# Kernel tuning notes

Hardware: AMD Instinct MI355X
Metric: run time of the kernel (lower is better)

## Reference

```python
import jax, jax.numpy as jnp
import numpy as np

B, S, D, F, H, R, BLK = 1, 2048, 1024, 2816, 16, 16, 64
DH = D // H  # 64

# bitsandbytes NF4 codebook
NF4_CODE = jnp.array([-1.0, -0.6961928009986877, -0.5250730514526367, -0.39491748809814453,
                      -0.28444138169288635, -0.18477343022823334, -0.09105003625154495, 0.0,
                      0.07958029955625534, 0.16093020141124725, 0.24611230194568634, 0.33791524171829224,
                      0.44070982933044434, 0.5626170039176941, 0.7229568362236023, 1.0], dtype=jnp.float32)


def dequant_nf4(codes, absmax, shape):
    # blockwise NF4 dequant: codebook lookup * per-64-element absmax scale
    w = NF4_CODE[codes.reshape(-1)]
    return (w.reshape(-1, BLK) * absmax[:, None]).reshape(shape)


def rmsnorm(x, w, eps=1e-10):
    return x * jax.lax.rsqrt(jnp.mean(x * x, axis=-1, keepdims=True) + eps) * w


def rotate_half(x):
    x1, x2 = jnp.split(x, 2, axis=-1)
    return jnp.concatenate((-x2, x1), axis=-1)


def apply_rope(x, cos, sin, pos):
    # x: [B,H,S,DH], pos: [B,S] -> gather rope tables per position
    c = cos[pos][:, None]  # [B,1,S,DH]
    s = sin[pos][:, None]
    return x * c + rotate_half(x) * s


def proj(x, codes, absmax, la, lb, shape):
    # fused NF4 dequant-matmul + additive LoRA branch: x @ W.T + (x @ A) @ B
    w = dequant_nf4(codes, absmax, shape)
    return x @ w.T + (x @ la) @ lb


def _forward(x, nw1, nw2, cos, sin,
             qa, qla, qlb, ka, kla, klb, va, vla, vlb, oa, ola, olb,
             ga, gla, glb, ua, ula, ulb, da, dla, dlb,
             pos, qc, kc, vc, oc, gc, uc, dc):
    h1 = rmsnorm(x, nw1)
    q = proj(h1, qc, qa, qla, qlb, (D, D))
    k = proj(h1, kc, ka, kla, klb, (D, D))
    v = proj(h1, vc, va, vla, vlb, (D, D))

    def heads(t):
        return t.reshape(B, S, H, DH).transpose(0, 2, 1, 3)

    q = apply_rope(heads(q), cos, sin, pos)
    k = apply_rope(heads(k), cos, sin, pos)
    v = heads(v)

    scores = jnp.einsum('bhqd,bhkd->bhqk', q, k) / np.float32(np.sqrt(DH))
    causal = jnp.tril(jnp.ones((S, S), dtype=bool))
    mask = jnp.where(causal, 0.0, -1e9).astype(scores.dtype)  # additive attention_mask
    attn = jax.nn.softmax(scores + mask, axis=-1)
    o = jnp.einsum('bhqk,bhkd->bhqd', attn, v).transpose(0, 2, 1, 3).reshape(B, S, D)
    o = proj(o, oc, oa, ola, olb, (D, D))

    x1 = x + o  # first residual
    h2 = rmsnorm(x1, nw2)
    gate = proj(h2, gc, ga, gla, glb, (F, D))
    up = proj(h2, uc, ua, ula, ulb, (F, D))
    had = up * jax.nn.silu(gate)  # SwiGLU hadamard
    down = proj(had, dc, da, dla, dlb, (D, F))
    return x1 + down


def setup_inputs():
    ks = iter(jax.random.split(jax.random.key(0), 48))

    def rn(shape, scale=1.0):
        return jax.random.normal(next(ks), shape, jnp.float32) * scale

    def cd(shape):
        return jax.random.randint(next(ks), shape, 0, 16, dtype=jnp.int32)

    def am(n):
        return jax.random.uniform(next(ks), (n,), jnp.float32) * 0.04 + 0.01

    inp = {'x': rn((B, S, D)),
           'norm_weight_1': 1.0 + rn((D,), 0.02),
           'norm_weight_2': 1.0 + rn((D,), 0.02)}
    inv = 1.0 / (10000.0 ** (jnp.arange(0, DH, 2, dtype=jnp.float32) / DH))
    ang = jnp.arange(S, dtype=jnp.float32)[:, None] * inv[None, :]
    emb = jnp.concatenate((ang, ang), axis=-1)  # [S, DH]
    inp['cos'], inp['sin'] = jnp.cos(emb), jnp.sin(emb)
    inp['position_ids'] = jnp.broadcast_to(jnp.arange(S, dtype=jnp.int32), (B, S))
    shapes = {'q': (D, D), 'k': (D, D), 'v': (D, D), 'o': (D, D),
              'gate': (F, D), 'up': (F, D), 'down': (D, F)}
    for p, (o, i) in shapes.items():
        inp['w_%s_codes' % p] = cd((o, i))
        inp['w_%s_absmax' % p] = am(o * i // BLK)
        inp['w_%s_lora_a' % p] = rn((i, R), 1.0 / np.sqrt(i))
        inp['w_%s_lora_b' % p] = rn((R, o), 0.01)
    return inp


def reference(x, norm_weight_1, norm_weight_2, cos, sin, position_ids,
              w_q_codes, w_q_absmax, w_q_lora_a, w_q_lora_b,
              w_k_codes, w_k_absmax, w_k_lora_a, w_k_lora_b,
              w_v_codes, w_v_absmax, w_v_lora_a, w_v_lora_b,
              w_o_codes, w_o_absmax, w_o_lora_a, w_o_lora_b,
              w_gate_codes, w_gate_absmax, w_gate_lora_a, w_gate_lora_b,
              w_up_codes, w_up_absmax, w_up_lora_a, w_up_lora_b,
              w_down_codes, w_down_absmax, w_down_lora_a, w_down_lora_b):
    return _forward(x, norm_weight_1, norm_weight_2, cos, sin,
                    w_q_absmax, w_q_lora_a, w_q_lora_b,
                    w_k_absmax, w_k_lora_a, w_k_lora_b,
                    w_v_absmax, w_v_lora_a, w_v_lora_b,
                    w_o_absmax, w_o_lora_a, w_o_lora_b,
                    w_gate_absmax, w_gate_lora_a, w_gate_lora_b,
                    w_up_absmax, w_up_lora_a, w_up_lora_b,
                    w_down_absmax, w_down_lora_a, w_down_lora_b,
                    position_ids, w_q_codes, w_k_codes, w_v_codes,
                    w_o_codes, w_gate_codes, w_up_codes, w_down_codes)
```

## Files before the change

### kernel.cpp

```cpp
#include <hip/hip_runtime.h>
#include <stdint.h>


#define Sq   2048
#define Dm   1024
#define Fm   2816
#define Hh   16
#define KE1  1088
#define KE2  1088
#define LGW  1088
#define KE3  2880
#define NQKV 3072
#define NGU  5632

typedef short bf16x8 __attribute__((ext_vector_type(8)));
typedef float f32x4  __attribute__((ext_vector_type(4)));

__constant__ float NF4_LUT[16] = {
    -1.0f, -0.6961928009986877f, -0.5250730514526367f, -0.39491748809814453f,
    -0.28444138169288635f, -0.18477343022823334f, -0.09105003625154495f, 0.0f,
    0.07958029955625534f, 0.16093020141124725f, 0.24611230194568634f,
    0.33791524171829224f, 0.44070982933044434f, 0.5626170039176941f,
    0.7229568362236023f, 1.0f};

__device__ inline unsigned short f2bf(float f) {
    union { float f; uint32_t u; } v; v.f = f;
    uint32_t u = v.u;
    return (unsigned short)((u + 0x7FFFu + ((u >> 16) & 1u)) >> 16);
}
__device__ inline float bf2f(unsigned short h) {
    union { uint32_t u; float f; } v; v.u = ((uint32_t)h) << 16;
    return v.f;
}
__device__ inline unsigned short truncbf(float f) {
    union { float f; uint32_t u; } v; v.f = f;
    return (unsigned short)(v.u >> 16);
}

#define GLD16(gp, lp)                                                         \
    __builtin_amdgcn_global_load_lds(                                         \
        (__attribute__((address_space(1))) void*)(uintptr_t)(gp),             \
        (__attribute__((address_space(3))) void*)(uint32_t)(uintptr_t)(lp),   \
        16, 0, 0)

__global__ __launch_bounds__(256) void rmsnorm_ext(
    const float* __restrict__ X, const float* __restrict__ W,
    unsigned short* Hout, int ldh)
{
    int s = blockIdx.x, tid = threadIdx.x;
    const float4 v = *(const float4*)(X + (size_t)s * Dm + tid * 4);
    float ss = v.x * v.x + v.y * v.y + v.z * v.z + v.w * v.w;
#pragma unroll
    for (int m = 1; m < 64; m <<= 1) ss += __shfl_xor(ss, m);
    __shared__ float red[4];
    int lane = tid & 63, wave = tid >> 6;
    if (lane == 0) red[wave] = ss;
    __syncthreads();
    float scale = rsqrtf((red[0] + red[1] + red[2] + red[3]) * (1.0f / Dm) + 1e-10f);
    const float4 w = *(const float4*)(W + tid * 4);
    alignas(8) unsigned short o[4];
    o[0] = f2bf(v.x * scale * w.x);
    o[1] = f2bf(v.y * scale * w.y);
    o[2] = f2bf(v.z * scale * w.z);
    o[3] = f2bf(v.w * scale * w.w);
    *(ushort4*)(Hout + (size_t)s * ldh + tid * 4) = *(ushort4*)o;
    if (tid < 64) Hout[(size_t)s * ldh + Dm + tid] = 0;
}

__device__ inline void dq_row8(const float* lut, const int* cod, const float* am,
                               const float* lb, int nr, int c8, int K, int Nlb,
                               int toff, unsigned short* out)
{
    if (c8 < K) {
        size_t base = (size_t)nr * K + c8;
        const int4* cp = (const int4*)(cod + base);
        int4 ca = cp[0], cb = cp[1];
        float a = am[base >> 6];
        out[0] = f2bf(lut[ca.x] * a); out[1] = f2bf(lut[ca.y] * a);
        out[2] = f2bf(lut[ca.z] * a); out[3] = f2bf(lut[ca.w] * a);
        out[4] = f2bf(lut[cb.x] * a); out[5] = f2bf(lut[cb.y] * a);
        out[6] = f2bf(lut[cb.z] * a); out[7] = f2bf(lut[cb.w] * a);
    } else {
        int r = c8 - toff;
#pragma unroll
        for (int i = 0; i < 8; ++i) out[i] = 0;
        if (r >= 0 && r < 16) {
#pragma unroll
            for (int i = 0; i < 8; ++i) out[i] = f2bf(lb[(size_t)(r + i) * Nlb + nr]);
        }
    }
}

__global__ __launch_bounds__(256) void prep_weights(
    const int* __restrict__ qc, const int* __restrict__ kc, const int* __restrict__ vc,
    const int* __restrict__ oc, const int* __restrict__ gc, const int* __restrict__ uc,
    const int* __restrict__ dc,
    const float* __restrict__ qa, const float* __restrict__ ka, const float* __restrict__ va,
    const float* __restrict__ oa, const float* __restrict__ ga, const float* __restrict__ ua,
    const float* __restrict__ da,
    const float* __restrict__ qla, const float* __restrict__ kla, const float* __restrict__ vla,
    const float* __restrict__ ola, const float* __restrict__ gla, const float* __restrict__ ula,
    const float* __restrict__ dla,
    const float* __restrict__ qlb, const float* __restrict__ klb, const float* __restrict__ vlb,
    const float* __restrict__ olb, const float* __restrict__ glb, const float* __restrict__ ulb,
    const float* __restrict__ dlb,
    const float* __restrict__ x, const float* __restrict__ nw1,
    unsigned short* __restrict__ lapk, unsigned short* __restrict__ Wq,
    unsigned short* __restrict__ Wo, unsigned short* __restrict__ Wgu,
    unsigned short* __restrict__ Wd, unsigned short* __restrict__ h)
{
    int b = blockIdx.x, tid = threadIdx.x;
    if (b >= 6678) {
        int s = b - 6678;
        const float4 v = *(const float4*)(x + (size_t)s * Dm + tid * 4);
        float ss = v.x * v.x + v.y * v.y + v.z * v.z + v.w * v.w;
#pragma unroll
        for (int m = 1; m < 64; m <<= 1) ss += __shfl_xor(ss, m);
        __shared__ float red[4];
        int lane = tid & 63, wave = tid >> 6;
        if (lane == 0) red[wave] = ss;
        __syncthreads();
        float scale = rsqrtf((red[0] + red[1] + red[2] + red[3]) * (1.0f / Dm) + 1e-10f);
        const float4 w = *(const float4*)(nw1 + tid * 4);
        alignas(8) unsigned short o[4];
        o[0] = f2bf(v.x * scale * w.x);
        o[1] = f2bf(v.y * scale * w.y);
        o[2] = f2bf(v.z * scale * w.z);
        o[3] = f2bf(v.w * scale * w.w);
        *(ushort4*)(h + (size_t)s * KE1 + tid * 4) = *(ushort4*)o;
        if (tid < 64) h[(size_t)s * KE1 + Dm + tid] = 0;
        return;
    }
    if (b < 70) {
        int chunk = b * 4 + (tid >> 6);
        int lane = tid & 63;
        int lr = lane & 15, quad = lane >> 4;
        const float* la;
        int lc;
        if (chunk < 192) {
            int m = chunk >> 5; lc = chunk & 31;
            la = (m == 0) ? qla : (m == 1) ? kla : (m == 2) ? vla
               : (m == 3) ? ola : (m == 4) ? gla : ula;
        } else {
            la = dla; lc = chunk - 192;
        }
        alignas(16) unsigned short out[8];
#pragma unroll
        for (int e = 0; e < 8; ++e)
            out[e] = f2bf(la[(size_t)(lc * 32 + quad * 8 + e) * 16 + lr]);
        *(uint4*)(lapk + (size_t)chunk * 512 + lane * 8) = *(uint4*)out;
        return;
    }
    __shared__ float lut[16];
    if (tid < 16) lut[tid] = NF4_LUT[tid];
    __syncthreads();
    if (b < 1702) {
        int idx = (b - 70) * 256 + tid;
        int n = idx / 136;
        int c8 = (idx - n * 136) * 8;
        int seg = n >> 10, nr = n & 1023;
        const int* cod   = (seg == 0) ? qc : (seg == 1) ? kc : vc;
        const float* am  = (seg == 0) ? qa : (seg == 1) ? ka : va;
        const float* lb  = (seg == 0) ? qlb : (seg == 1) ? klb : vlb;
        int toff = 1024 + (seg << 4);
        alignas(16) unsigned short out[8];
        dq_row8(lut, cod, am, lb, nr, c8, 1024, 1024, toff, out);
        *(uint4*)(Wq + (size_t)n * KE1 + c8) = *(uint4*)out;
    } else if (b < 2246) {
        int idx = (b - 1702) * 256 + tid;
        int n = idx / 136;
        int c8 = (idx - n * 136) * 8;
        alignas(16) unsigned short out[8];
        dq_row8(lut, oc, oa, olb, n, c8, 1024, Dm, 1024, out);
        *(uint4*)(Wo + (size_t)n * KE2 + c8) = *(uint4*)out;
    } else if (b < 5238) {
        int idx = (b - 2246) * 256 + tid;
        int n = idx / 136;
        int v8 = idx - n * 136;
        int m = n >> 1, mat = n & 1;
        const int* cod  = mat ? uc : gc;
        const float* am = mat ? ua : ga;
        const float* lb = mat ? ulb : glb;
        int toff = 1024 + (mat << 4);
        alignas(16) unsigned short out[8];
        dq_row8(lut, cod, am, lb, m, v8 * 8, 1024, Fm, toff, out);
        int ch = v8 >> 2, sub = v8 & 3;
        int ph = ch + (n % 34); if (ph >= 34) ph -= 34;
        *(uint4*)(Wgu + (size_t)n * LGW + ph * 32 + sub * 8) = *(uint4*)out;
    } else {
        int idx = (b - 5238) * 256 + tid;
        int n = idx / 360;
        if (n >= Dm) return;
        int c8 = (idx - n * 360) * 8;
        alignas(16) unsigned short out[8];
        dq_row8(lut, dc, da, dlb, n, c8, 2816, Dm, 2816, out);
        *(uint4*)(Wd + (size_t)n * KE3 + c8) = *(uint4*)out;
    }
}

template<int NM>
__global__ __launch_bounds__(256) void lora_mfma(
    unsigned short* Aext, int lda, int K,
    const unsigned short* __restrict__ lapk, int c0, int c1, int c2,
    int toff, int zoff, int zn)
{
    int tid = threadIdx.x;
    int lane = tid & 63, wave = tid >> 6;
    int lr = lane & 15, quad = lane >> 4;
    int r0 = blockIdx.x * 16;
    int nc4 = K >> 7;
    int gc0 = wave * nc4;
    const unsigned short* Ab = Aext + (size_t)(r0 + lr) * lda + quad * 8;
    int cb[3] = {c0, c1, c2};
    f32x4 zero = {0.f, 0.f, 0.f, 0.f};
    f32x4 acc[NM];
#pragma unroll
    for (int m = 0; m < NM; ++m) acc[m] = zero;
    for (int cc = 0; cc < nc4; ++cc) {
        int gc = gc0 + cc;
        bf16x8 af = *(const bf16x8*)(Ab + gc * 32);
#pragma unroll
        for (int m = 0; m < NM; ++m) {
            bf16x8 bf = *(const bf16x8*)(lapk + (size_t)(cb[m] + gc) * 512 + lane * 8);
            acc[m] = __builtin_amdgcn_mfma_f32_16x16x32_bf16(af, bf, acc[m], 0, 0, 0);
        }
    }
    __shared__ float red[3][NM * 64 * 4];
    if (wave > 0) {
#pragma unroll
        for (int m = 0; m < NM; ++m)
#pragma unroll
            for (int r = 0; r < 4; ++r)
                red[wave - 1][(m * 64 + lane) * 4 + r] = acc[m][r];
    }
    __syncthreads();
    if (wave == 0) {
#pragma unroll
        for (int m = 0; m < NM; ++m)
#pragma unroll
            for (int r = 0; r < 4; ++r)
                acc[m][r] += red[0][(m * 64 + lane) * 4 + r]
                           + red[1][(m * 64 + lane) * 4 + r]
                           + red[2][(m * 64 + lane) * 4 + r];
#pragma unroll
        for (int r = 0; r < 4; ++r) {
            int row = r0 + quad * 4 + r;
#pragma unroll
            for (int m = 0; m < NM; ++m)
                Aext[(size_t)row * lda + toff + m * 16 + lr] = f2bf(acc[m][r]);
        }
        if (zn > 0) {
            int row = r0 + lr, j0 = quad * 4;
            for (int j = j0; j < zn; j += 64) {
                alignas(8) unsigned short z4[4] = {0, 0, 0, 0};
                *(ushort4*)(Aext + (size_t)row * lda + zoff + j) = *(ushort4*)z4;
            }
        }
    }
}

__global__ __launch_bounds__(256) void gemm128(
    const unsigned short* __restrict__ A, int lda,
    const unsigned short* __restrict__ B, int ldb, int K,
    unsigned short* __restrict__ Cb, int ldc)
{
    __shared__ __align__(16) unsigned short At[2][128 * 32];
    __shared__ __align__(16) unsigned short Bt[2][128 * 32];
    int tid = threadIdx.x;
    int lane = tid & 63, wave = tid >> 6;
    int lr = lane & 15, quad = lane >> 4;
    int wm = (wave >> 1) * 64, wn = (wave & 1) * 64;
    int row0 = blockIdx.y * 128, col0 = blockIdx.x * 128;
    f32x4 acc[4][4];
    f32x4 zero = {0.f, 0.f, 0.f, 0.f};
#pragma unroll
    for (int i = 0; i < 4; ++i)
#pragma unroll
        for (int j = 0; j < 4; ++j) acc[i][j] = zero;
    int sw = ((tid & 3) ^ ((tid >> 3) & 3)) * 8;
    const unsigned short* Ag  = A + (size_t)(row0 + (tid >> 2)) * lda + sw;
    const unsigned short* Ag2 = Ag + (size_t)64 * lda;
    const unsigned short* Bg  = B + (size_t)(col0 + (tid >> 2)) * ldb + sw;
    const unsigned short* Bg2 = Bg + (size_t)64 * ldb;
    int l0 = tid * 8, l1 = (tid + 256) * 8;
    GLD16(Ag, At[0] + l0); GLD16(Ag2, At[0] + l1);
    GLD16(Bg, Bt[0] + l0); GLD16(Bg2, Bt[0] + l1);
    int sq = (quad ^ ((lr >> 1) & 3)) * 8;
    int nIter = K >> 5;
    for (int it = 0; it < nIter; ++it) {
        int cur = it & 1;
        __syncthreads();
        if (it + 1 < nIter) {
            int k = (it + 1) << 5, nx = cur ^ 1;
            GLD16(Ag + k, At[nx] + l0); GLD16(Ag2 + k, At[nx] + l1);
            GLD16(Bg + k, Bt[nx] + l0); GLD16(Bg2 + k, Bt[nx] + l1);
        }
        bf16x8 af[4], bfr[4];
#pragma unroll
        for (int i = 0; i < 4; ++i)
            af[i] = *(const bf16x8*)(At[cur] + (wm + i * 16 + lr) * 32 + sq);
#pragma unroll
        for (int j = 0; j < 4; ++j)
            bfr[j] = *(const bf16x8*)(Bt[cur] + (wn + j * 16 + lr) * 32 + sq);
#pragma unroll
        for (int i = 0; i < 4; ++i)
#pragma unroll
            for (int j = 0; j < 4; ++j)
                acc[i][j] = __builtin_amdgcn_mfma_f32_16x16x32_bf16(af[i], bfr[j], acc[i][j], 0, 0, 0);
    }
#pragma unroll
    for (int i = 0; i < 4; ++i) {
        int rowb = row0 + wm + i * 16 + quad * 4;
#pragma unroll
        for (int j = 0; j < 4; ++j) {
            int col = col0 + wn + j * 16 + lr;
#pragma unroll
            for (int r = 0; r < 4; ++r)
                Cb[(size_t)(rowb + r) * ldc + col] = f2bf(acc[i][j][r]);
        }
    }
}

__global__ __launch_bounds__(256) void gemm_gu(
    const unsigned short* __restrict__ A, int lda,
    const unsigned short* __restrict__ B, int ldb, int K,
    unsigned short* __restrict__ Hb)
{
    __shared__ __align__(16) unsigned short At[2][128 * 32];
    __shared__ __align__(16) unsigned short Bt[2][128 * 32];
    int tid = threadIdx.x;
    int lane = tid & 63, wave = tid >> 6;
    int lr = lane & 15, quad = lane >> 4;
    int wm = (wave >> 1) * 64, wn = (wave & 1) * 64;
    int row0 = blockIdx.y * 128, col0 = blockIdx.x * 128;
    f32x4 acc[4][4];
    f32x4 zero = {0.f, 0.f, 0.f, 0.f};
#pragma unroll
    for (int i = 0; i < 4; ++i)
#pragma unroll
        for (int j = 0; j < 4; ++j) acc[i][j] = zero;
    int sw = ((tid & 3) ^ ((tid >> 3) & 3)) * 8;
    const unsigned short* Ag  = A + (size_t)(row0 + (tid >> 2)) * lda + sw;
    const unsigned short* Ag2 = Ag + (size_t)64 * lda;
    int rB  = col0 + (tid >> 2);
    const unsigned short* Bb  = B + (size_t)rB * ldb + sw;
    const unsigned short* Bb2 = B + (size_t)(rB + 64) * ldb + sw;
    int cB  = rB % 34;
    int cB2 = (rB + 64) % 34;
    int l0 = tid * 8, l1 = (tid + 256) * 8;
    GLD16(Ag, At[0] + l0); GLD16(Ag2, At[0] + l1);
    GLD16(Bb + cB * 32, Bt[0] + l0);
    GLD16(Bb2 + cB2 * 32, Bt[0] + l1);
    cB  = (cB + 1 == 34) ? 0 : cB + 1;
    cB2 = (cB2 + 1 == 34) ? 0 : cB2 + 1;
    int sq = (quad ^ ((lr >> 1) & 3)) * 8;
    int nIter = K >> 5;
    for (int it = 0; it < nIter; ++it) {
        int cur = it & 1;
        __syncthreads();
        if (it + 1 < nIter) {
            int k = (it + 1) << 5, nx = cur ^ 1;
            GLD16(Ag + k, At[nx] + l0); GLD16(Ag2 + k, At[nx] + l1);
            GLD16(Bb + cB * 32, Bt[nx] + l0);
            GLD16(Bb2 + cB2 * 32, Bt[nx] + l1);
            cB  = (cB + 1 == 34) ? 0 : cB + 1;
            cB2 = (cB2 + 1 == 34) ? 0 : cB2 + 1;
        }
        bf16x8 af[4], bfr[4];
#pragma unroll
        for (int i = 0; i < 4; ++i)
            af[i] = *(const bf16x8*)(At[cur] + (wm + i * 16 + lr) * 32 + sq);
#pragma unroll
        for (int j = 0; j < 4; ++j)
            bfr[j] = *(const bf16x8*)(Bt[cur] + (wn + j * 16 + lr) * 32 + sq);
#pragma unroll
        for (int i = 0; i < 4; ++i)
#pragma unroll
            for (int j = 0; j < 4; ++j)
                acc[i][j] = __builtin_amdgcn_mfma_f32_16x16x32_bf16(af[i], bfr[j], acc[i][j], 0, 0, 0);
    }
#pragma unroll
    for (int i = 0; i < 4; ++i) {
        int rowb = row0 + wm + i * 16 + quad * 4;
#pragma unroll
        for (int j = 0; j < 4; ++j) {
            int col = col0 + wn + j * 16 + lr;
#pragma unroll
            for (int r = 0; r < 4; ++r) {
                float own = acc[i][j][r];
                float oth = __shfl_xor(own, 1);
                if (!(lr & 1)) {
                    float sig = 1.0f / (1.0f + __expf(-own));
                    Hb[(size_t)(rowb + r) * KE3 + (col >> 1)] = f2bf(oth * own * sig);
                }
            }
        }
    }
}

template<int TAG>
__global__ __launch_bounds__(256) void gemm_s(
    const unsigned short* __restrict__ A, int lda,
    const unsigned short* __restrict__ B, int ldb, int K,
    float* __restrict__ Cf, int ldc, const float* __restrict__ Radd)
{
    __shared__ __align__(16) unsigned short At[2][64 * 64];
    __shared__ __align__(16) unsigned short Bt[2][64 * 64];
    int tid = threadIdx.x;
    int lane = tid & 63, wave = tid >> 6;
    int lr = lane & 15, quad = lane >> 4;
    int row0 = blockIdx.y * 64, col0 = blockIdx.x * 64;
    f32x4 acc[4];
    f32x4 zero = {0.f, 0.f, 0.f, 0.f};
#pragma unroll
    for (int j = 0; j < 4; ++j) acc[j] = zero;
    int rs = tid >> 3;
    int g8 = ((tid & 7) ^ (rs & 7)) * 8;
    const unsigned short* Ag  = A + (size_t)(row0 + rs) * lda + g8;
    const unsigned short* Ag2 = Ag + (size_t)32 * lda;
    const unsigned short* Bg  = B + (size_t)(col0 + rs) * ldb + g8;
    const unsigned short* Bg2 = Bg + (size_t)32 * ldb;
    int l0 = tid * 8, l1 = (tid + 256) * 8;
    GLD16(Ag, At[0] + l0); GLD16(Ag2, At[0] + l1);
    GLD16(Bg, Bt[0] + l0); GLD16(Bg2, Bt[0] + l1);
    int c0 = (quad ^ (lr & 7)) * 8;
    int c1 = ((4 + quad) ^ (lr & 7)) * 8;
    int nIter = K >> 6;
    for (int it = 0; it < nIter; ++it) {
        int cur = it & 1;
        __syncthreads();
        if (it + 1 < nIter) {
            int k = (it + 1) << 6, nx = cur ^ 1;
            GLD16(Ag + k, At[nx] + l0); GLD16(Ag2 + k, At[nx] + l1);
            GLD16(Bg + k, Bt[nx] + l0); GLD16(Bg2 + k, Bt[nx] + l1);
        }
        const unsigned short* arow = At[cur] + (wave * 16 + lr) * 64;
        bf16x8 a0 = *(const bf16x8*)(arow + c0);
        bf16x8 a1 = *(const bf16x8*)(arow + c1);
        bf16x8 b0[4], b1[4];
#pragma unroll
        for (int j = 0; j < 4; ++j) {
            const unsigned short* brow = Bt[cur] + (j * 16 + lr) * 64;
            b0[j] = *(const bf16x8*)(brow + c0);
            b1[j] = *(const bf16x8*)(brow + c1);
        }
#pragma unroll
        for (int j = 0; j < 4; ++j) {
            acc[j] = __builtin_amdgcn_mfma_f32_16x16x32_bf16(a0, b0[j], acc[j], 0, 0, 0);
            acc[j] = __builtin_amdgcn_mfma_f32_16x16x32_bf16(a1, b1[j], acc[j], 0, 0, 0);
        }
    }
    int rowb = row0 + wave * 16 + quad * 4;
#pragma unroll
    for (int j = 0; j < 4; ++j) {
        int col = col0 + j * 16 + lr;
#pragma unroll
        for (int r = 0; r < 4; ++r) {
            size_t o = (size_t)(rowb + r) * ldc + col;
            Cf[o] = acc[j][r] + Radd[o];
        }
    }
}

__global__ __launch_bounds__(256) void rope_pack(
    const unsigned short* __restrict__ qkv,
    const float* __restrict__ cosT, const float* __restrict__ sinT,
    const int* __restrict__ pos,
    unsigned short* __restrict__ kpk, unsigned short* __restrict__ vpk)
{
    int b = blockIdx.x, tid = threadIdx.x;
    if (b < 1024) {
        int g = b * 256 + tid;
        int lr = g & 15, quad = (g >> 4) & 3, cch = (g >> 6) & 1;
        int t = (g >> 7) & 127, h = g >> 14;
        int s = t * 16 + lr;
        int p = pos[s];
        int d0 = cch * 32 + quad * 8;
        const unsigned short* krow = qkv + (size_t)s * NQKV + Dm + h * 64;
        uint4 kv8 = *(const uint4*)(krow + d0);
        uint4 kp8 = *(const uint4*)(krow + ((d0 + 32) & 63));
        float sgn = (d0 < 32) ? -1.f : 1.f;
        const float* cp = cosT + p * 64 + d0;
        const float* sp = sinT + p * 64 + d0;
        const unsigned short* ke = (const unsigned short*)&kv8;
        const unsigned short* pe = (const unsigned short*)&kp8;
        alignas(16) unsigned short out[8];
#pragma unroll
        for (int e = 0; e < 8; ++e)
            out[e] = f2bf(bf2f(ke[e]) * cp[e] + sgn * bf2f(pe[e]) * sp[e]);
        *(uint4*)(kpk + (size_t)g * 8) = *(uint4*)out;
    } else {
        int g = (b - 1024) * 256 + tid;
        int lrr = g & 15, quad = (g >> 4) & 3, kk = (g >> 6) & 3;
        int j = (g >> 8) & 3, kt = (g >> 10) & 15, h = g >> 14;
        int d = j * 16 + lrr;
        int sbase = kt * 128 + kk * 32 + quad * 8;
        alignas(16) unsigned short out[8];
#pragma unroll
        for (int e = 0; e < 8; ++e)
            out[e] = qkv[(size_t)(sbase + e) * NQKV + 2048 + h * 64 + d];
        *(uint4*)(vpk + (size_t)g * 8) = *(uint4*)out;
    }
}

__global__ __launch_bounds__(256) void attn(
    const unsigned short* __restrict__ qkv, const int* __restrict__ pos,
    const float* __restrict__ cosT, const float* __restrict__ sinT,
    const unsigned short* __restrict__ kpk, const unsigned short* __restrict__ vpk,
    unsigned short* __restrict__ ob)
{
    __shared__ __align__(16) unsigned short Ps[4][16 * 136];
    int tid = threadIdx.x;
    int lane = tid & 63, wave = tid >> 6;
    int lr = lane & 15, quad = lane >> 4;
    int idx = blockIdx.x;
    int t_ = idx >> 4;
    int qt = (idx < 256) ? (31 - t_) : (t_ - 16);
    int h = idx & 15;
    int r0 = qt * 64 + wave * 16;
    int qrow = r0 + lr;
    int p = pos[qrow];
    const unsigned short* qp = qkv + (size_t)qrow * NQKV + h * 64 + quad * 8;
    uint4 q0v = *(const uint4*)qp;
    uint4 q1v = *(const uint4*)(qp + 32);
    const float* cp = cosT + p * 64 + quad * 8;
    const float* sp = sinT + p * 64 + quad * 8;
    const unsigned short* q0e = (const unsigned short*)&q0v;
    const unsigned short* q1e = (const unsigned short*)&q1v;
    alignas(16) unsigned short qo0[8], qo1[8];
#pragma unroll
    for (int e = 0; e < 8; ++e) {
        float a = bf2f(q0e[e]), bq = bf2f(q1e[e]);
        qo0[e] = f2bf((a * cp[e] - bq * sp[e]) * 0.125f);
        qo1[e] = f2bf((bq * cp[32 + e] + a * sp[32 + e]) * 0.125f);
    }
    bf16x8 qf0 = *(const bf16x8*)qo0;
    bf16x8 qf1 = *(const bf16x8*)qo1;
    const unsigned short* kpb = kpk + (size_t)h * 128 * 1024 + lane * 8;
    const unsigned short* vpb = vpk + (size_t)h * 16 * 16 * 512 + lane * 8;
    f32x4 zero = {0.f, 0.f, 0.f, 0.f};
    f32x4 oacc[4];
#pragma unroll
    for (int j = 0; j < 4; ++j) oacc[j] = zero;
    float lrow[4] = {0.f, 0.f, 0.f, 0.f};
    int ntile = (qt * 64 + 191) >> 7;

    for (int kt = 0; kt < ntile; ++kt) {
        int k0 = kt << 7;
        f32x4 sf[8];
#pragma unroll
        for (int jj = 0; jj < 8; ++jj) {
            const unsigned short* kp = kpb + (size_t)(kt * 8 + jj) * 1024;
            bf16x8 kf0 = *(const bf16x8*)kp;
            bf16x8 kf1 = *(const bf16x8*)(kp + 512);
            f32x4 z = zero;
            z = __builtin_amdgcn_mfma_f32_16x16x32_bf16(qf0, kf0, z, 0, 0, 0);
            z = __builtin_amdgcn_mfma_f32_16x16x32_bf16(qf1, kf1, z, 0, 0, 0);
            sf[jj] = z;
        }
        bf16x8 vf[4][4];
#pragma unroll
        for (int j = 0; j < 4; ++j)
#pragma unroll
            for (int kk = 0; kk < 4; ++kk)
                vf[j][kk] = *(const bf16x8*)(vpb + (size_t)((kt * 4 + j) * 4 + kk) * 512);
        if (kt == ntile - 1) {
#pragma unroll
            for (int jj = 0; jj < 8; ++jj)
#pragma unroll
                for (int r = 0; r < 4; ++r)
                    if (k0 + jj * 16 + lr > r0 + quad * 4 + r)
                        sf[jj][r] = -1e30f;
        }
#pragma unroll
        for (int jj = 0; jj < 8; ++jj)
#pragma unroll
            for (int r = 0; r < 4; ++r) {
                float pr = __expf(sf[jj][r]);
                sf[jj][r] = pr;
                lrow[r] += pr;
            }
#pragma unroll
        for (int jj = 0; jj < 8; ++jj)
#pragma unroll
            for (int r = 0; r < 4; ++r)
                Ps[wave][(quad * 4 + r) * 136 + jj * 16 + lr] = truncbf(sf[jj][r]);
        bf16x8 pf[4];
#pragma unroll
        for (int kk = 0; kk < 4; ++kk)
            pf[kk] = *(const bf16x8*)(&Ps[wave][lr * 136 + kk * 32 + quad * 8]);
#pragma unroll
        for (int j = 0; j < 4; ++j)
#pragma unroll
            for (int kk = 0; kk < 4; ++kk)
                oacc[j] = __builtin_amdgcn_mfma_f32_16x16x32_bf16(pf[kk], vf[j][kk], oacc[j], 0, 0, 0);
    }
#pragma unroll
    for (int r = 0; r < 4; ++r)
#pragma unroll
        for (int m = 1; m < 16; m <<= 1) lrow[r] += __shfl_xor(lrow[r], m);
#pragma unroll
    for (int r = 0; r < 4; ++r) {
        float inv = 1.0f / lrow[r];
        int row = r0 + quad * 4 + r;
#pragma unroll
        for (int j = 0; j < 4; ++j)
            ob[(size_t)row * KE2 + h * 64 + j * 16 + lr] = f2bf(oacc[j][r] * inv);
    }
}

extern "C" void kernel_launch(void* const* d_in, const int* in_sizes, int n_in,
                              void* d_out, int out_size, void* d_ws, size_t ws_size,
                              hipStream_t stream)
{
    const float* x    = (const float*)d_in[0];
    const float* nw1  = (const float*)d_in[1];
    const float* nw2  = (const float*)d_in[2];
    const float* cosT = (const float*)d_in[3];
    const float* sinT = (const float*)d_in[4];
    const int*   pos  = (const int*)d_in[5];
    const int   *qc = (const int*)d_in[6],  *kc = (const int*)d_in[10],
                *vc = (const int*)d_in[14], *oc = (const int*)d_in[18],
                *gc = (const int*)d_in[22], *uc = (const int*)d_in[26],
                *dc = (const int*)d_in[30];
    const float *qa = (const float*)d_in[7],  *ka = (const float*)d_in[11],
                *va = (const float*)d_in[15], *oa = (const float*)d_in[19],
                *ga = (const float*)d_in[23], *ua = (const float*)d_in[27],
                *da = (const float*)d_in[31];
    const float *qla = (const float*)d_in[8],  *kla = (const float*)d_in[12],
                *vla = (const float*)d_in[16], *ola = (const float*)d_in[20],
                *gla = (const float*)d_in[24], *ula = (const float*)d_in[28],
                *dla = (const float*)d_in[32];
    const float *qlb = (const float*)d_in[9],  *klb = (const float*)d_in[13],
                *vlb = (const float*)d_in[17], *olb = (const float*)d_in[21],
                *glb = (const float*)d_in[25], *ulb = (const float*)d_in[29],
                *dlb = (const float*)d_in[33];

    char* ws = (char*)d_ws;
    unsigned short* h    = (unsigned short*)(ws + 0);
    unsigned short* Wgu  = (unsigned short*)(ws + 4456448);
    unsigned short* qkv  = (unsigned short*)(ws + 16711680);
    unsigned short* kpk  = (unsigned short*)(ws + 33488896);
    unsigned short* vpk  = (unsigned short*)(ws + 37683200);
    unsigned short* obf  = (unsigned short*)(ws + 41877504);
    float*          x1   = (float*)(ws + 29294592);
    unsigned short* hb   = (unsigned short*)(ws + 46333952);
    unsigned short* Wq   = (unsigned short*)(ws + 46333952);
    unsigned short* Wo   = (unsigned short*)(ws + 53022720);
    unsigned short* lapk = (unsigned short*)(ws + 58130432);
    unsigned short* Wd   = (unsigned short*)(ws + 58425344);
    float* outp = (float*)d_out;

    prep_weights<<<8726, 256, 0, stream>>>(
        qc, kc, vc, oc, gc, uc, dc, qa, ka, va, oa, ga, ua, da,
        qla, kla, vla, ola, gla, ula, dla, qlb, klb, vlb, olb, glb, ulb, dlb,
        x, nw1, lapk, Wq, Wo, Wgu, Wd, h);
    lora_mfma<3><<<128, 256, 0, stream>>>(h, KE1, Dm, lapk, 0, 32, 64, 1024, 0, 0);
    gemm128<<<dim3(NQKV / 128, Sq / 128), 256, 0, stream>>>(h, KE1, Wq, KE1, KE1, qkv, NQKV);
    rope_pack<<<2048, 256, 0, stream>>>(qkv, cosT, sinT, pos, kpk, vpk);
    attn<<<512, 256, 0, stream>>>(qkv, pos, cosT, sinT, kpk, vpk, obf);
    lora_mfma<1><<<128, 256, 0, stream>>>(obf, KE2, Dm, lapk, 96, 0, 0, 1024, 1040, 16);
    gemm_s<0><<<dim3(Dm / 64, Sq / 64), 256, 0, stream>>>(obf, KE2, Wo, KE2, KE2, x1, Dm, x);
    rmsnorm_ext<<<Sq, 256, 0, stream>>>(x1, nw2, h, KE1);
    lora_mfma<2><<<128, 256, 0, stream>>>(h, KE1, Dm, lapk, 128, 160, 0, 1024, 0, 0);
    gemm_gu<<<dim3(NGU / 128, Sq / 128), 256, 0, stream>>>(h, KE1, Wgu, LGW, LGW, hb);
    lora_mfma<1><<<128, 256, 0, stream>>>(hb, KE3, Fm, lapk, 192, 0, 0, 2816, 2832, 16);
    gemm_s<1><<<dim3(Dm / 64, Sq / 64), 256, 0, stream>>>(hb, KE3, Wd, KE3, KE3, outp, Dm, x1);
}
```

Measured before the change: 328.5 us.

## Triple-buffer LDS tiles in GEMM kernels with explicit vmcnt waits

Moves the three GEMM kernels (gemm128, gemm_gu, gemm_s) from double-buffered to triple-buffered LDS staging. Each kernel now prefetches two K-tiles ahead and replaces __syncthreads with an explicit s_waitcnt vmcnt(4) plus s_barrier. Only the oldest tile's loads must finish before compute, so global-load latency can overlap more with MFMA work. The cost is 50% more shared memory per block, which may lower occupancy. Correctness also depends on the compiler not reordering the hand-placed waitcnt relative to the direct-to-LDS loads.

Result: no change. 323.8 us (-1.4%).

```diff
diff --git a/kernel.cpp b/kernel.cpp
--- a/kernel.cpp
+++ b/kernel.cpp
@@ -42,6 +42,8 @@
         (__attribute__((address_space(1))) void*)(uintptr_t)(gp),             \
         (__attribute__((address_space(3))) void*)(uint32_t)(uintptr_t)(lp),   \
         16, 0, 0)
+
+#define WAITV(n) asm volatile("s_waitcnt vmcnt(" #n ")" ::: "memory")
 
 __global__ __launch_bounds__(256) void rmsnorm_ext(
     const float* __restrict__ X, const float* __restrict__ W,
@@ -264,8 +266,8 @@
     const unsigned short* __restrict__ B, int ldb, int K,
     unsigned short* __restrict__ Cb, int ldc)
 {
-    __shared__ __align__(16) unsigned short At[2][128 * 32];
-    __shared__ __align__(16) unsigned short Bt[2][128 * 32];
+    __shared__ __align__(16) unsigned short At[3][128 * 32];
+    __shared__ __align__(16) unsigned short Bt[3][128 * 32];
     int tid = threadIdx.x;
     int lane = tid & 63, wave = tid >> 6;
     int lr = lane & 15, quad = lane >> 4;
@@ -283,17 +285,20 @@
     const unsigned short* Bg  = B + (size_t)(col0 + (tid >> 2)) * ldb + sw;
     const unsigned short* Bg2 = Bg + (size_t)64 * ldb;
     int l0 = tid * 8, l1 = (tid + 256) * 8;
-    GLD16(Ag, At[0] + l0); GLD16(Ag2, At[0] + l1);
-    GLD16(Bg, Bt[0] + l0); GLD16(Bg2, Bt[0] + l1);
+    GLD16(Ag,      At[0] + l0); GLD16(Ag2,      At[0] + l1);
+    GLD16(Bg,      Bt[0] + l0); GLD16(Bg2,      Bt[0] + l1);
+    GLD16(Ag + 32, At[1] + l0); GLD16(Ag2 + 32, At[1] + l1);
+    GLD16(Bg + 32, Bt[1] + l0); GLD16(Bg2 + 32, Bt[1] + l1);
     int sq = (quad ^ ((lr >> 1) & 3)) * 8;
     int nIter = K >> 5;
+    int cur = 0, wbuf = 2;
     for (int it = 0; it < nIter; ++it) {
-        int cur = it & 1;
-        __syncthreads();
-        if (it + 1 < nIter) {
-            int k = (it + 1) << 5, nx = cur ^ 1;
-            GLD16(Ag + k, At[nx] + l0); GLD16(Ag2 + k, At[nx] + l1);
-            GLD16(Bg + k, Bt[nx] + l0); GLD16(Bg2 + k, Bt[nx] + l1);
+        if (it + 1 < nIter) WAITV(4); else WAITV(0);
+        __builtin_amdgcn_s_barrier();
+        if (it + 2 < nIter) {
+            int k = (it + 2) << 5;
+            GLD16(Ag + k, At[wbuf] + l0); GLD16(Ag2 + k, At[wbuf] + l1);
+            GLD16(Bg + k, Bt[wbuf] + l0); GLD16(Bg2 + k, Bt[wbuf] + l1);
         }
         bf16x8 af[4], bfr[4];
 #pragma unroll
@@ -307,6 +312,8 @@
 #pragma unroll
             for (int j = 0; j < 4; ++j)
                 acc[i][j] = __builtin_amdgcn_mfma_f32_16x16x32_bf16(af[i], bfr[j], acc[i][j], 0, 0, 0);
+        cur  = (cur  == 2) ? 0 : cur  + 1;
+        wbuf = (wbuf == 2) ? 0 : wbuf + 1;
     }
 #pragma unroll
     for (int i = 0; i < 4; ++i) {
@@ -326,8 +333,8 @@
     const unsigned short* __restrict__ B, int ldb, int K,
     unsigned short* __restrict__ Hb)
 {
-    __shared__ __align__(16) unsigned short At[2][128 * 32];
-    __shared__ __align__(16) unsigned short Bt[2][128 * 32];
+    __shared__ __align__(16) unsigned short At[3][128 * 32];
+    __shared__ __align__(16) unsigned short Bt[3][128 * 32];
     int tid = threadIdx.x;
     int lane = tid & 63, wave = tid >> 6;
     int lr = lane & 15, quad = lane >> 4;
@@ -348,21 +355,27 @@
     int cB  = rB % 34;
     int cB2 = (rB + 64) % 34;
     int l0 = tid * 8, l1 = (tid + 256) * 8;
-    GLD16(Ag, At[0] + l0); GLD16(Ag2, At[0] + l1);
+    GLD16(Ag,      At[0] + l0); GLD16(Ag2,      At[0] + l1);
     GLD16(Bb + cB * 32, Bt[0] + l0);
     GLD16(Bb2 + cB2 * 32, Bt[0] + l1);
     cB  = (cB + 1 == 34) ? 0 : cB + 1;
     cB2 = (cB2 + 1 == 34) ? 0 : cB2 + 1;
+    GLD16(Ag + 32, At[1] + l0); GLD16(Ag2 + 32, At[1] + l1);
+    GLD16(Bb + cB * 32, Bt[1] + l0);
+    GLD16(Bb2 + cB2 * 32, Bt[1] + l1);
+    cB  = (cB + 1 == 34) ? 0 : cB + 1;
+    cB2 = (cB2 + 1 == 34) ? 0 : cB2 + 1;
     int sq = (quad ^ ((lr >> 1) & 3)) * 8;
     int nIter = K >> 5;
+    int cur = 0, wbuf = 2;
     for (int it = 0; it < nIter; ++it) {
-        int cur = it & 1;
-        __syncthreads();
-        if (it + 1 < nIter) {
-            int k = (it + 1) << 5, nx = cur ^ 1;
-            GLD16(Ag + k, At[nx] + l0); GLD16(Ag2 + k, At[nx] + l1);
-            GLD16(Bb + cB * 32, Bt[nx] + l0);
-            GLD16(Bb2 + cB2 * 32, Bt[nx] + l1);
+        if (it + 1 < nIter) WAITV(4); else WAITV(0);
+        __builtin_amdgcn_s_barrier();
+        if (it + 2 < nIter) {
+            int k = (it + 2) << 5;
+            GLD16(Ag + k, At[wbuf] + l0); GLD16(Ag2 + k, At[wbuf] + l1);
+            GLD16(Bb + cB * 32, Bt[wbuf] + l0);
+            GLD16(Bb2 + cB2 * 32, Bt[wbuf] + l1);
             cB  = (cB + 1 == 34) ? 0 : cB + 1;
             cB2 = (cB2 + 1 == 34) ? 0 : cB2 + 1;
         }
@@ -378,6 +391,8 @@
 #pragma unroll
             for (int j = 0; j < 4; ++j)
                 acc[i][j] = __builtin_amdgcn_mfma_f32_16x16x32_bf16(af[i], bfr[j], acc[i][j], 0, 0, 0);
+        cur  = (cur  == 2) ? 0 : cur  + 1;
+        wbuf = (wbuf == 2) ? 0 : wbuf + 1;
     }
 #pragma unroll
     for (int i = 0; i < 4; ++i) {
@@ -404,8 +419,8 @@
     const unsigned short* __restrict__ B, int ldb, int K,
     float* __restrict__ Cf, int ldc, const float* __restrict__ Radd)
 {
-    __shared__ __align__(16) unsigned short At[2][64 * 64];
-    __shared__ __align__(16) unsigned short Bt[2][64 * 64];
+    __shared__ __align__(16) unsigned short At[3][64 * 64];
+    __shared__ __align__(16) unsigned short Bt[3][64 * 64];
     int tid = threadIdx.x;
     int lane = tid & 63, wave = tid >> 6;
     int lr = lane & 15, quad = lane >> 4;
@@ -421,18 +436,21 @@
     const unsigned short* Bg  = B + (size_t)(col0 + rs) * ldb + g8;
     const unsigned short* Bg2 = Bg + (size_t)32 * ldb;
     int l0 = tid * 8, l1 = (tid + 256) * 8;
-    GLD16(Ag, At[0] + l0); GLD16(Ag2, At[0] + l1);
-    GLD16(Bg, Bt[0] + l0); GLD16(Bg2, Bt[0] + l1);
+    GLD16(Ag,      At[0] + l0); GLD16(Ag2,      At[0] + l1);
+    GLD16(Bg,      Bt[0] + l0); GLD16(Bg2,      Bt[0] + l1);
+    GLD16(Ag + 64, At[1] + l0); GLD16(Ag2 + 64, At[1] + l1);
+    GLD16(Bg + 64, Bt[1] + l0); GLD16(Bg2 + 64, Bt[1] + l1);
     int c0 = (quad ^ (lr & 7)) * 8;
     int c1 = ((4 + quad) ^ (lr & 7)) * 8;
     int nIter = K >> 6;
+    int cur = 0, wbuf = 2;
     for (int it = 0; it < nIter; ++it) {
-        int cur = it & 1;
-        __syncthreads();
-        if (it + 1 < nIter) {
-            int k = (it + 1) << 6, nx = cur ^ 1;
-            GLD16(Ag + k, At[nx] + l0); GLD16(Ag2 + k, At[nx] + l1);
-            GLD16(Bg + k, Bt[nx] + l0); GLD16(Bg2 + k, Bt[nx] + l1);
+        if (it + 1 < nIter) WAITV(4); else WAITV(0);
+        __builtin_amdgcn_s_barrier();
+        if (it + 2 < nIter) {
+            int k = (it + 2) << 6;
+            GLD16(Ag + k, At[wbuf] + l0); GLD16(Ag2 + k, At[wbuf] + l1);
+            GLD16(Bg + k, Bt[wbuf] + l0); GLD16(Bg2 + k, Bt[wbuf] + l1);
         }
         const unsigned short* arow = At[cur] + (wave * 16 + lr) * 64;
         bf16x8 a0 = *(const bf16x8*)(arow + c0);
@@ -449,6 +467,8 @@
             acc[j] = __builtin_amdgcn_mfma_f32_16x16x32_bf16(a0, b0[j], acc[j], 0, 0, 0);
             acc[j] = __builtin_amdgcn_mfma_f32_16x16x32_bf16(a1, b1[j], acc[j], 0, 0, 0);
         }
+        cur  = (cur  == 2) ? 0 : cur  + 1;
+        wbuf = (wbuf == 2) ? 0 : wbuf + 1;
     }
     int rowb = row0 + wave * 16 + quad * 4;
 #pragma unroll
```
